# Optimization experiments

Measured on AMD Instinct MI355X. Metric: run time of the kernel, lower is better.

Reference implementation:

```python
import jax, jax.numpy as jnp
import numpy as np

B, S, D = 2, 2048, 1024
M = 2048          # d_mlp
E = 8             # num_experts
TOP_K = 2


def setup_inputs() -> dict:
    key = jax.random.key(0)
    ks = jax.random.split(key, 5)
    std = 0.02
    return {
        "residual": jax.random.normal(ks[0], (B, S, D), jnp.float32),
        "W_router": jax.random.normal(ks[1], (D, E), jnp.float32) * std,
        "W_gate": jax.random.normal(ks[2], (E, D, M), jnp.float32) * std,
        "b_gate": jnp.zeros((E, M), jnp.float32),
        "W_up": jax.random.normal(ks[3], (E, D, M), jnp.float32) * std,
        "b_up": jnp.zeros((E, M), jnp.float32),
        "W_out": jax.random.normal(ks[4], (E, M, D), jnp.float32) * std,
        "b_out": jnp.zeros((E, D), jnp.float32),
    }


def reference(residual, W_router, W_gate, b_gate, W_up, b_up, W_out, b_out):
    # --- router: softmax over experts, top-k selection, renormalize ---
    router_logits = jnp.einsum('bsd,de->bse', residual, W_router)
    router_probs = jax.nn.softmax(router_logits, axis=-1)
    top_k_probs, top_k_idx = jax.lax.top_k(router_probs, TOP_K)          # [B,S,K]
    top_k_probs = top_k_probs / (jnp.sum(top_k_probs, -1, keepdims=True) + 1e-8)
    # per-expert combine weight [B,S,E]; top-k indices are unique per token
    one_hot = jax.nn.one_hot(top_k_idx, E, dtype=residual.dtype)          # [B,S,K,E]
    expert_weights = jnp.einsum('bsk,bske->bse', top_k_probs, one_hot)
    # --- each expert runs dense SwiGLU MLP on the FULL batch (compute-then-mask, as in source) ---
    gate = jax.nn.silu(jnp.einsum('bsd,edm->ebsm', residual, W_gate) + b_gate[:, None, None, :])
    up = jnp.einsum('bsd,edm->ebsm', residual, W_up) + b_up[:, None, None, :]
    hidden = gate * up                                                    # [E,B,S,M]
    expert_out = jnp.einsum('ebsm,emd->ebsd', hidden, W_out) + b_out[:, None, None, :]
    # --- weighted combine (weights are zero for non-selected experts) ---
    output = jnp.einsum('bse,ebsd->bsd', expert_weights, expert_out)
    return output
```

## Files before the change

### kernel.cpp

```cpp
#include <hip/hip_runtime.h>
#include <cstdint>
#include <cstddef>

#define TT 4096
#define DD 1024
#define MM 2048
#define EE 8
#define NPAIR 8192

typedef unsigned short u16;
typedef __bf16 bf16x8 __attribute__((ext_vector_type(8)));
typedef float f32x4 __attribute__((ext_vector_type(4)));
typedef u16 u16x8 __attribute__((ext_vector_type(8)));
typedef __attribute__((address_space(3))) void* lds_vp;
typedef __attribute__((address_space(1))) const void* gbl_cvp;

__device__ __forceinline__ void async16(u16* l, const u16* g) {
  __builtin_amdgcn_global_load_lds((gbl_cvp)(const void*)g, (lds_vp)(void*)l, 16, 0, 0);
}

__device__ __forceinline__ u16 f2bf(float f) {
  uint32_t u = __builtin_bit_cast(uint32_t, f);
  u += 0x7fffu + ((u >> 16) & 1u);
  return (u16)(u >> 16);
}
__device__ __forceinline__ float bf2f(u16 h) {
  uint32_t u = ((uint32_t)h) << 16;
  return __builtin_bit_cast(float, u);
}

__global__ void router_kernel(const float* __restrict__ X, const float* __restrict__ Wr,
                              int* __restrict__ tok_idx, float* __restrict__ wpair,
                              u16* __restrict__ Xbf) {
  int wave = threadIdx.x >> 6;
  int lane = threadIdx.x & 63;
  int t = blockIdx.x * 4 + wave;
  const float4* x4 = (const float4*)(X + (size_t)t * DD);
  float acc[EE];
#pragma unroll
  for (int e = 0; e < EE; e++) acc[e] = 0.f;
#pragma unroll
  for (int i = 0; i < 4; i++) {
    float4 xv = x4[i * 64 + lane];
    ushort4 o;
    o.x = f2bf(xv.x); o.y = f2bf(xv.y); o.z = f2bf(xv.z); o.w = f2bf(xv.w);
    *(ushort4*)&Xbf[(size_t)t * DD + (size_t)(i * 64 + lane) * 4] = o;
    const float4* wr4 = (const float4*)(Wr + (size_t)(i * 256 + lane * 4) * EE);
    float xs[4] = {xv.x, xv.y, xv.z, xv.w};
#pragma unroll
    for (int c = 0; c < 4; c++) {
      float4 wa = wr4[c * 2 + 0];
      float4 wb = wr4[c * 2 + 1];
      acc[0] += xs[c] * wa.x; acc[1] += xs[c] * wa.y;
      acc[2] += xs[c] * wa.z; acc[3] += xs[c] * wa.w;
      acc[4] += xs[c] * wb.x; acc[5] += xs[c] * wb.y;
      acc[6] += xs[c] * wb.z; acc[7] += xs[c] * wb.w;
    }
  }
#pragma unroll
  for (int off = 32; off > 0; off >>= 1)
#pragma unroll
    for (int e = 0; e < EE; e++) acc[e] += __shfl_xor(acc[e], off);
  if (lane == 0) {
    float mx = acc[0];
#pragma unroll
    for (int e = 1; e < EE; e++) mx = fmaxf(mx, acc[e]);
    float p[EE], s = 0.f;
#pragma unroll
    for (int e = 0; e < EE; e++) { p[e] = __expf(acc[e] - mx); s += p[e]; }
    float inv = 1.f / s;
#pragma unroll
    for (int e = 0; e < EE; e++) p[e] *= inv;
    int i0 = 0;
#pragma unroll
    for (int e = 1; e < EE; e++) if (p[e] > p[i0]) i0 = e;
    int i1 = (i0 == 0) ? 1 : 0;
#pragma unroll
    for (int e = 0; e < EE; e++) if (e != i0 && p[e] > p[i1]) i1 = e;
    float denom = p[i0] + p[i1] + 1e-8f;
    tok_idx[t * 2 + 0] = i0;
    tok_idx[t * 2 + 1] = i1;
    wpair[t * 2 + 0] = p[i0] / denom;
    wpair[t * 2 + 1] = p[i1] / denom;
  }
}

__global__ void bucket_kernel(const int* __restrict__ tok_idx, int* __restrict__ offsets,
                              int* __restrict__ bucket) {
  __shared__ int lcnt[EE];
  __shared__ int lcur[EE];
  int tid = threadIdx.x;
  if (tid < EE) lcnt[tid] = 0;
  __syncthreads();
  for (int i = tid; i < NPAIR; i += 1024) atomicAdd(&lcnt[tok_idx[i]], 1);
  __syncthreads();
  if (tid == 0) {
    int s = 0;
    for (int e = 0; e < EE; e++) {
      offsets[e] = s;
      lcur[e] = s;
      s += lcnt[e];
    }
    offsets[EE] = s;
  }
  __syncthreads();
  for (int i = tid; i < NPAIR; i += 1024) {
    int e = tok_idx[i];
    int pos = atomicAdd(&lcur[e], 1);
    bucket[pos] = i;
  }
}

__global__ __launch_bounds__(256)
void transpose_cvt(const float* __restrict__ in, u16* __restrict__ out, int R, int C) {
  __shared__ float tile[64][65];
  int e = blockIdx.z;
  const float* I = in + (size_t)e * R * C;
  u16* O = out + (size_t)e * R * C;
  int c0 = blockIdx.x * 64, r0 = blockIdx.y * 64;
  int t = threadIdx.x;
  {
    int cq = t & 15;
    int rb = t >> 4;
#pragma unroll
    for (int i = 0; i < 4; i++) {
      int r = rb + i * 16;
      float4 v = *(const float4*)&I[(size_t)(r0 + r) * C + c0 + cq * 4];
      tile[cq * 4 + 0][r] = v.x;
      tile[cq * 4 + 1][r] = v.y;
      tile[cq * 4 + 2][r] = v.z;
      tile[cq * 4 + 3][r] = v.w;
    }
  }
  __syncthreads();
  {
    int rseg = (t & 7) * 8;
    int cc = t >> 3;
#pragma unroll
    for (int i = 0; i < 2; i++) {
      int c = cc + i * 32;
      u16x8 o;
#pragma unroll
      for (int k = 0; k < 8; k++) o[k] = f2bf(tile[c][rseg + k]);
      *(u16x8*)&O[(size_t)(c0 + c) * R + r0 + rseg] = o;
    }
  }
}

__device__ __forceinline__ bool tile_map(const int* __restrict__ offsets, int x,
                                         int& expert, int& row0, int& rows) {
  expert = -1;
#pragma unroll 1
  for (int e = 0; e < EE; e++) {
    int o0 = offsets[e], o1 = offsets[e + 1];
    int nt = (o1 - o0 + 127) >> 7;
    if (x < nt) { expert = e; row0 = o0 + (x << 7); rows = min(128, o1 - row0); return true; }
    x -= nt;
  }
  return false;
}

template <int NTLOG2>
__device__ __forceinline__ void grid_decode(int bid, int& rt, int& n0) {
  int xcd = bid & 7, slot = bid >> 3;
  rt = xcd * 9 + (slot >> NTLOG2);
  n0 = (slot & ((1 << NTLOG2) - 1)) * 128;
}


__global__ __launch_bounds__(256, 2)
void moe_gemm_gu(const u16* __restrict__ Xbf, const u16* __restrict__ WtG,
                 const u16* __restrict__ WtU, const float* __restrict__ bgate,
                 const float* __restrict__ bup, u16* __restrict__ Hws,
                 const int* __restrict__ offsets, const int* __restrict__ bucket) {
  int rt, n0;
  grid_decode<4>(blockIdx.x, rt, n0);
  int expert, row0, rows;
  if (!tile_map(offsets, rt, expert, row0, rows)) return;

  __shared__ u16 Alds[2][128 * 32];
  __shared__ u16 Glds[2][128 * 32];
  __shared__ u16 Ulds[2][128 * 32];

  int tid = threadIdx.x;
  int wave = tid >> 6, lane = tid & 63;
  int wm = wave >> 1, wn = wave & 1;
  int quad = lane >> 4, l15 = lane & 15;
  int swz = ((lane & 3) ^ ((lane >> 3) & 3)) * 8;
  int rp  = (quad ^ ((l15 >> 1) & 3)) * 8;

  long arow0, arow1;
  {
    int r0l = wave * 32 + (lane >> 2);
    int rr0 = min(r0l, rows - 1);
    int rr1 = min(r0l + 16, rows - 1);
    arow0 = (long)(bucket[row0 + rr0] >> 1) * DD;
    arow1 = (long)(bucket[row0 + rr1] >> 1) * DD;
  }
  const u16* A0 = Xbf + arow0 + swz;
  const u16* A1 = Xbf + arow1 + swz;
  size_t bo = (size_t)expert * MM * DD + (size_t)n0 * DD
            + (long)(wave * 32 + (lane >> 2)) * DD + swz;
  const u16* G0 = WtG + bo; const u16* G1 = G0 + 16 * DD;
  const u16* U0 = WtU + bo; const u16* U1 = U0 + 16 * DD;

  int sb0 = (wave * 32) * 32, sb1 = (wave * 32 + 16) * 32;

  f32x4 accG[4][4], accU[4][4];
#pragma unroll
  for (int i = 0; i < 4; i++)
#pragma unroll
    for (int j = 0; j < 4; j++) { accG[i][j] = (f32x4){0,0,0,0}; accU[i][j] = (f32x4){0,0,0,0}; }

  auto stage = [&](int b) {
    async16(&Alds[b][sb0], A0); async16(&Alds[b][sb1], A1);
    async16(&Glds[b][sb0], G0); async16(&Glds[b][sb1], G1);
    async16(&Ulds[b][sb0], U0); async16(&Ulds[b][sb1], U1);
    A0 += 32; A1 += 32; G0 += 32; G1 += 32; U0 += 32; U1 += 32;
  };

  stage(0);
  __syncthreads();

  constexpr int NT = DD / 32;
#pragma unroll 2
  for (int t = 0; t < NT; ++t) {
    int cur = t & 1;
    if (t + 1 < NT) stage(cur ^ 1);
    bf16x8 af[4], bf[4];
#pragma unroll
    for (int i = 0; i < 4; i++) {
      af[i] = *(const bf16x8*)&Alds[cur][(wm * 64 + i * 16 + l15) * 32 + rp];
      bf[i] = *(const bf16x8*)&Glds[cur][(wn * 64 + i * 16 + l15) * 32 + rp];
    }
#pragma unroll
    for (int i = 0; i < 4; i++)
#pragma unroll
      for (int j = 0; j < 4; j++)
        accG[i][j] = __builtin_amdgcn_mfma_f32_16x16x32_bf16(af[i], bf[j], accG[i][j], 0, 0, 0);
#pragma unroll
    for (int i = 0; i < 4; i++)
      bf[i] = *(const bf16x8*)&Ulds[cur][(wn * 64 + i * 16 + l15) * 32 + rp];
#pragma unroll
    for (int i = 0; i < 4; i++)
#pragma unroll
      for (int j = 0; j < 4; j++)
        accU[i][j] = __builtin_amdgcn_mfma_f32_16x16x32_bf16(af[i], bf[j], accU[i][j], 0, 0, 0);
    __syncthreads();
  }

#pragma unroll
  for (int i = 0; i < 4; i++) {
    int lrb = wm * 64 + i * 16 + quad * 4;
#pragma unroll
    for (int j = 0; j < 4; j++) {
      int gc = n0 + wn * 64 + j * 16 + l15;
      float bg = bgate[expert * MM + gc];
      float bu = bup[expert * MM + gc];
#pragma unroll
      for (int r = 0; r < 4; r++) {
        int lr = lrb + r;
        if (lr < rows) {
          int grow = row0 + lr;
          float g = accG[i][j][r] + bg;
          float u = accU[i][j][r] + bu;
          float sg = g / (1.f + __expf(-g));
          Hws[(size_t)grow * MM + gc] = f2bf(sg * u);
        }
      }
    }
  }
}

__global__ __launch_bounds__(256)
void moe_gemm_out(const u16* __restrict__ Hmat, const u16* __restrict__ WtO,
                  const float* __restrict__ bias, float* __restrict__ Ypart,
                  const int* __restrict__ offsets, const int* __restrict__ bucket,
                  const float* __restrict__ wpair) {
  int rt, n0;
  grid_decode<3>(blockIdx.x, rt, n0);
  int expert, row0, rows;
  if (!tile_map(offsets, rt, expert, row0, rows)) return;

  __shared__ u16 Alds[2][128 * 32];
  __shared__ u16 Blds[2][128 * 32];

  int tid = threadIdx.x;
  int wave = tid >> 6, lane = tid & 63;
  int wm = wave >> 1, wn = wave & 1;
  int quad = lane >> 4, l15 = lane & 15;
  int swz = ((lane & 3) ^ ((lane >> 3) & 3)) * 8;
  int rp  = (quad ^ ((l15 >> 1) & 3)) * 8;

  long arow0, arow1;
  {
    int r0l = wave * 32 + (lane >> 2);
    int rr0 = min(r0l, rows - 1);
    int rr1 = min(r0l + 16, rows - 1);
    arow0 = (long)(row0 + rr0) * MM;
    arow1 = (long)(row0 + rr1) * MM;
  }
  const u16* A0 = Hmat + arow0 + swz;
  const u16* A1 = Hmat + arow1 + swz;
  const u16* B0 = WtO + (size_t)expert * DD * MM + (size_t)n0 * MM
                + (long)(wave * 32 + (lane >> 2)) * MM + swz;
  const u16* B1 = B0 + 16 * MM;

  int sb0 = (wave * 32) * 32, sb1 = (wave * 32 + 16) * 32;

  f32x4 acc[4][4];
#pragma unroll
  for (int i = 0; i < 4; i++)
#pragma unroll
    for (int j = 0; j < 4; j++) acc[i][j] = (f32x4){0, 0, 0, 0};

  auto stage = [&](int b) {
    async16(&Alds[b][sb0], A0); async16(&Alds[b][sb1], A1);
    async16(&Blds[b][sb0], B0); async16(&Blds[b][sb1], B1);
    A0 += 32; A1 += 32; B0 += 32; B1 += 32;
  };

  stage(0);
  __syncthreads();

  constexpr int NT = MM / 32;
#pragma unroll 2
  for (int t = 0; t < NT; ++t) {
    int cur = t & 1;
    if (t + 1 < NT) stage(cur ^ 1);
    bf16x8 af[4], bf[4];
#pragma unroll
    for (int i = 0; i < 4; i++) {
      af[i] = *(const bf16x8*)&Alds[cur][(wm * 64 + i * 16 + l15) * 32 + rp];
      bf[i] = *(const bf16x8*)&Blds[cur][(wn * 64 + i * 16 + l15) * 32 + rp];
    }
#pragma unroll
    for (int i = 0; i < 4; i++)
#pragma unroll
      for (int j = 0; j < 4; j++)
        acc[i][j] = __builtin_amdgcn_mfma_f32_16x16x32_bf16(af[i], bf[j], acc[i][j], 0, 0, 0);
    __syncthreads();
  }

#pragma unroll
  for (int i = 0; i < 4; i++) {
    int lrb = wm * 64 + i * 16 + quad * 4;
#pragma unroll
    for (int j = 0; j < 4; j++) {
      int gc = n0 + wn * 64 + j * 16 + l15;
      float bv = bias[expert * DD + gc];
#pragma unroll
      for (int r = 0; r < 4; r++) {
        int lr = lrb + r;
        if (lr < rows) {
          int grow = row0 + lr;
          int p = bucket[grow];
          float w = wpair[p];
          Ypart[(size_t)p * DD + gc] = w * (acc[i][j][r] + bv);
        }
      }
    }
  }
}

__global__ void combine_kernel(const float* __restrict__ Ypart, float* __restrict__ out) {
  int i = blockIdx.x * 256 + threadIdx.x;
  int t = i >> 8;
  int c4 = i & 255;
  const float4* y0 = (const float4*)(Ypart + (size_t)(2 * t) * DD) + c4;
  const float4* y1 = (const float4*)(Ypart + (size_t)(2 * t + 1) * DD) + c4;
  float4 a = *y0, b = *y1;
  float4 o;
  o.x = a.x + b.x; o.y = a.y + b.y; o.z = a.z + b.z; o.w = a.w + b.w;
  ((float4*)out)[i] = o;
}

extern "C" void kernel_launch(void* const* d_in, const int* in_sizes, int n_in,
                              void* d_out, int out_size, void* d_ws, size_t ws_size,
                              hipStream_t stream) {
  const float* residual = (const float*)d_in[0];
  const float* W_router = (const float*)d_in[1];
  const float* W_gate   = (const float*)d_in[2];
  const float* b_gate   = (const float*)d_in[3];
  const float* W_up     = (const float*)d_in[4];
  const float* b_up     = (const float*)d_in[5];
  const float* W_out    = (const float*)d_in[6];
  const float* b_out    = (const float*)d_in[7];
  float* out = (float*)d_out;

  char* ws = (char*)d_ws;
  int*   tok_idx = (int*)(ws + 0);
  float* wpair   = (float*)(ws + 32768);
  int*   offsets = (int*)(ws + 65536);
  int*   bucket  = (int*)(ws + 65536 + 512);
  u16*   Xbf  = (u16*)(ws + 131072);
  u16*   WtG  = Xbf + (size_t)TT * DD;
  u16*   WtU  = WtG + (size_t)EE * MM * DD;
  u16*   WtO  = WtU + (size_t)EE * MM * DD;
  u16*   Hws  = WtO + (size_t)EE * DD * MM;
  float* Ypart = (float*)(Hws + (size_t)NPAIR * MM);

  router_kernel<<<dim3(TT / 4), dim3(256), 0, stream>>>(residual, W_router, tok_idx, wpair, Xbf);
  bucket_kernel<<<dim3(1), dim3(1024), 0, stream>>>(tok_idx, offsets, bucket);
  transpose_cvt<<<dim3(MM / 64, DD / 64, EE), dim3(256), 0, stream>>>(W_gate, WtG, DD, MM);
  transpose_cvt<<<dim3(MM / 64, DD / 64, EE), dim3(256), 0, stream>>>(W_up,   WtU, DD, MM);
  transpose_cvt<<<dim3(DD / 64, MM / 64, EE), dim3(256), 0, stream>>>(W_out,  WtO, MM, DD);
  moe_gemm_gu<<<dim3(8 * 9 * 16), dim3(256), 0, stream>>>(Xbf, WtG, WtU, b_gate, b_up, Hws, offsets, bucket);
  moe_gemm_out<<<dim3(8 * 9 * 8), dim3(256), 0, stream>>>(Hws, WtO, b_out, Ypart, offsets, bucket, wpair);
  combine_kernel<<<dim3(TT * DD / 4 / 256), dim3(256), 0, stream>>>(Ypart, out);
}
```

Baseline: 467.8 us.

## Triple-buffer MoE GEMM LDS pipeline with vmcnt waits and setprio; ballot-based bucketing

Both expert GEMM kernels move from a double-buffered loop with a full __syncthreads per step to a three-stage ring buffer. Each step waits only for the oldest in-flight async loads (vmcnt), then issues a single barrier, so two tiles of global loads stay in flight while MFMAs run. MFMA blocks are wrapped in s_setprio, and the output GEMM gets a 3-waves-per-SIMD launch bound. The bucket kernel replaces per-element LDS atomics with wave ballot/popcount aggregation; this costs extra LDS (a third buffer) and may lower occupancy.

Result: no change. 468.0 us (+0.0%).

```diff
diff --git a/kernel.cpp b/kernel.cpp
--- a/kernel.cpp
+++ b/kernel.cpp
@@ -18,6 +18,11 @@
 __device__ __forceinline__ void async16(u16* l, const u16* g) {
   __builtin_amdgcn_global_load_lds((gbl_cvp)(const void*)g, (lds_vp)(void*)l, 16, 0, 0);
 }
+
+#define VMCNT6() asm volatile("s_waitcnt vmcnt(6)" ::: "memory")
+#define VMCNT4() asm volatile("s_waitcnt vmcnt(4)" ::: "memory")
+#define VMCNT0() asm volatile("s_waitcnt vmcnt(0)" ::: "memory")
+#define BARR() do { asm volatile("" ::: "memory"); __builtin_amdgcn_s_barrier(); asm volatile("" ::: "memory"); } while (0)
 
 __device__ __forceinline__ u16 f2bf(float f) {
   uint32_t u = __builtin_bit_cast(uint32_t, f);
@@ -90,9 +95,27 @@
   __shared__ int lcnt[EE];
   __shared__ int lcur[EE];
   int tid = threadIdx.x;
+  int lane = tid & 63;
   if (tid < EE) lcnt[tid] = 0;
   __syncthreads();
-  for (int i = tid; i < NPAIR; i += 1024) atomicAdd(&lcnt[tok_idx[i]], 1);
+  {
+    int cnt[EE];
+#pragma unroll
+    for (int k = 0; k < EE; k++) cnt[k] = 0;
+    for (int i = tid; i < NPAIR; i += 1024) {
+      int e = tok_idx[i];
+#pragma unroll
+      for (int k = 0; k < EE; k++) {
+        unsigned long long m = __ballot(e == k);
+        cnt[k] += __popcll(m);
+      }
+    }
+    if (lane == 0) {
+#pragma unroll
+      for (int k = 0; k < EE; k++)
+        if (cnt[k]) atomicAdd(&lcnt[k], cnt[k]);
+    }
+  }
   __syncthreads();
   if (tid == 0) {
     int s = 0;
@@ -106,7 +129,19 @@
   __syncthreads();
   for (int i = tid; i < NPAIR; i += 1024) {
     int e = tok_idx[i];
-    int pos = atomicAdd(&lcur[e], 1);
+    int pos = 0;
+#pragma unroll
+    for (int k = 0; k < EE; k++) {
+      unsigned long long m = __ballot(e == k);
+      int c = __popcll(m);
+      if (c) {
+        int leader = (int)__ffsll((long long)m) - 1;
+        int base = 0;
+        if (lane == leader) base = atomicAdd(&lcur[k], c);
+        base = __shfl(base, leader);
+        if (e == k) pos = base + __popcll(m & ((1ull << lane) - 1ull));
+      }
+    }
     bucket[pos] = i;
   }
 }
@@ -178,9 +213,9 @@
   int expert, row0, rows;
   if (!tile_map(offsets, rt, expert, row0, rows)) return;
 
-  __shared__ u16 Alds[2][128 * 32];
-  __shared__ u16 Glds[2][128 * 32];
-  __shared__ u16 Ulds[2][128 * 32];
+  __shared__ u16 Alds[3 * 128 * 32];
+  __shared__ u16 Glds[3 * 128 * 32];
+  __shared__ u16 Ulds[3 * 128 * 32];
 
   int tid = threadIdx.x;
   int wave = tid >> 6, lane = tid & 63;
@@ -213,41 +248,54 @@
     for (int j = 0; j < 4; j++) { accG[i][j] = (f32x4){0,0,0,0}; accU[i][j] = (f32x4){0,0,0,0}; }
 
   auto stage = [&](int b) {
-    async16(&Alds[b][sb0], A0); async16(&Alds[b][sb1], A1);
-    async16(&Glds[b][sb0], G0); async16(&Glds[b][sb1], G1);
-    async16(&Ulds[b][sb0], U0); async16(&Ulds[b][sb1], U1);
+    int bo2 = b * (128 * 32);
+    async16(&Alds[bo2 + sb0], A0); async16(&Alds[bo2 + sb1], A1);
+    async16(&Glds[bo2 + sb0], G0); async16(&Glds[bo2 + sb1], G1);
+    async16(&Ulds[bo2 + sb0], U0); async16(&Ulds[bo2 + sb1], U1);
     A0 += 32; A1 += 32; G0 += 32; G1 += 32; U0 += 32; U1 += 32;
   };
 
-  stage(0);
-  __syncthreads();
-
-  constexpr int NT = DD / 32;
-#pragma unroll 2
-  for (int t = 0; t < NT; ++t) {
-    int cur = t & 1;
-    if (t + 1 < NT) stage(cur ^ 1);
+  auto compute = [&](int b) {
+    int ro = b * (128 * 32);
     bf16x8 af[4], bf[4];
 #pragma unroll
     for (int i = 0; i < 4; i++) {
-      af[i] = *(const bf16x8*)&Alds[cur][(wm * 64 + i * 16 + l15) * 32 + rp];
-      bf[i] = *(const bf16x8*)&Glds[cur][(wn * 64 + i * 16 + l15) * 32 + rp];
-    }
+      af[i] = *(const bf16x8*)&Alds[ro + (wm * 64 + i * 16 + l15) * 32 + rp];
+      bf[i] = *(const bf16x8*)&Glds[ro + (wn * 64 + i * 16 + l15) * 32 + rp];
+    }
+    __builtin_amdgcn_s_setprio(1);
 #pragma unroll
     for (int i = 0; i < 4; i++)
 #pragma unroll
       for (int j = 0; j < 4; j++)
         accG[i][j] = __builtin_amdgcn_mfma_f32_16x16x32_bf16(af[i], bf[j], accG[i][j], 0, 0, 0);
+    __builtin_amdgcn_s_setprio(0);
 #pragma unroll
     for (int i = 0; i < 4; i++)
-      bf[i] = *(const bf16x8*)&Ulds[cur][(wn * 64 + i * 16 + l15) * 32 + rp];
+      bf[i] = *(const bf16x8*)&Ulds[ro + (wn * 64 + i * 16 + l15) * 32 + rp];
+    __builtin_amdgcn_s_setprio(1);
 #pragma unroll
     for (int i = 0; i < 4; i++)
 #pragma unroll
       for (int j = 0; j < 4; j++)
         accU[i][j] = __builtin_amdgcn_mfma_f32_16x16x32_bf16(af[i], bf[j], accU[i][j], 0, 0, 0);
-    __syncthreads();
-  }
+    __builtin_amdgcn_s_setprio(0);
+  };
+
+  constexpr int NT = DD / 32;
+  stage(0);
+  stage(1);
+  int br = 0, bs = 2;
+#pragma unroll 1
+  for (int t = 0; t < NT - 2; ++t) {
+    VMCNT6();
+    BARR();
+    stage(bs);
+    compute(br);
+    bs = br; br = (br + 1 == 3) ? 0 : br + 1;
+  }
+  VMCNT6(); BARR(); compute(br); br = (br + 1 == 3) ? 0 : br + 1;
+  VMCNT0(); BARR(); compute(br);
 
 #pragma unroll
   for (int i = 0; i < 4; i++) {
@@ -272,7 +320,7 @@
   }
 }
 
-__global__ __launch_bounds__(256)
+__global__ __launch_bounds__(256, 3)
 void moe_gemm_out(const u16* __restrict__ Hmat, const u16* __restrict__ WtO,
                   const float* __restrict__ bias, float* __restrict__ Ypart,
                   const int* __restrict__ offsets, const int* __restrict__ bucket,
@@ -282,8 +330,8 @@
   int expert, row0, rows;
   if (!tile_map(offsets, rt, expert, row0, rows)) return;
 
-  __shared__ u16 Alds[2][128 * 32];
-  __shared__ u16 Blds[2][128 * 32];
+  __shared__ u16 Alds[3 * 128 * 32];
+  __shared__ u16 Blds[3 * 128 * 32];
 
   int tid = threadIdx.x;
   int wave = tid >> 6, lane = tid & 63;
@@ -315,32 +363,43 @@
     for (int j = 0; j < 4; j++) acc[i][j] = (f32x4){0, 0, 0, 0};
 
   auto stage = [&](int b) {
-    async16(&Alds[b][sb0], A0); async16(&Alds[b][sb1], A1);
-    async16(&Blds[b][sb0], B0); async16(&Blds[b][sb1], B1);
+    int bo2 = b * (128 * 32);
+    async16(&Alds[bo2 + sb0], A0); async16(&Alds[bo2 + sb1], A1);
+    async16(&Blds[bo2 + sb0], B0); async16(&Blds[bo2 + sb1], B1);
     A0 += 32; A1 += 32; B0 += 32; B1 += 32;
   };
 
-  stage(0);
-  __syncthreads();
-
-  constexpr int NT = MM / 32;
-#pragma unroll 2
-  for (int t = 0; t < NT; ++t) {
-    int cur = t & 1;
-    if (t + 1 < NT) stage(cur ^ 1);
+  auto compute = [&](int b) {
+    int ro = b * (128 * 32);
     bf16x8 af[4], bf[4];
 #pragma unroll
     for (int i = 0; i < 4; i++) {
-      af[i] = *(const bf16x8*)&Alds[cur][(wm * 64 + i * 16 + l15) * 32 + rp];
-      bf[i] = *(const bf16x8*)&Blds[cur][(wn * 64 + i * 16 + l15) * 32 + rp];
-    }
+      af[i] = *(const bf16x8*)&Alds[ro + (wm * 64 + i * 16 + l15) * 32 + rp];
+      bf[i] = *(const bf16x8*)&Blds[ro + (wn * 64 + i * 16 + l15) * 32 + rp];
+    }
+    __builtin_amdgcn_s_setprio(1);
 #pragma unroll
     for (int i = 0; i < 4; i++)
 #pragma unroll
       for (int j = 0; j < 4; j++)
         acc[i][j] = __builtin_amdgcn_mfma_f32_16x16x32_bf16(af[i], bf[j], acc[i][j], 0, 0, 0);
-    __syncthreads();
-  }
+    __builtin_amdgcn_s_setprio(0);
+  };
+
+  constexpr int NT = MM / 32;
+  stage(0);
+  stage(1);
+  int br = 0, bs = 2;
+#pragma unroll 1
+  for (int t = 0; t < NT - 2; ++t) {
+    VMCNT4();
+    BARR();
+    stage(bs);
+    compute(br);
+    bs = br; br = (br + 1 == 3) ? 0 : br + 1;
+  }
+  VMCNT4(); BARR(); compute(br); br = (br + 1 == 3) ? 0 : br + 1;
+  VMCNT0(); BARR(); compute(br);
 
 #pragma unroll
   for (int i = 0; i < 4; i++) {
```
